# Kernel optimization log

Measured on AMD Instinct MI355X. Metric: run time of the kernel, lower is better.

The kernel has to match this reference:

```python
import jax, jax.numpy as jnp
import numpy as np
import itertools

N, F, R, O, OUT = 131072, 32, 256, 5, 100
K = 9  # 2*exp_param + 1 with exp_param=4


def setup_inputs() -> dict:
    key = jax.random.key(0)
    k1, k2, k3 = jax.random.split(key, 3)
    # binary features -> get_route(x)==1 -> categorical rule path
    x = jax.random.randint(k1, (N, F), 0, 2).astype(jnp.float32)
    # first R combinations of O feature indices out of F (itertools order, as in __init__)
    combs = np.array(list(itertools.islice(itertools.combinations(range(F), O), R)), dtype=np.int32)
    comb_space = jax.random.normal(k2, (O, R), dtype=jnp.float32)
    w_out = jax.random.normal(k3, (OUT, R), dtype=jnp.float32) * 0.05
    b_out = jnp.zeros((OUT,), jnp.float32)
    return {"x": x, "comb_space": comb_space, "w_out": w_out, "b_out": b_out,
            "comb_idx": jnp.asarray(combs)}


def reference(x, comb_space, w_out, b_out, comb_idx):
    # Fused version of the per-rule Python loop:
    # gather all rule feature subsets at once: [N, R, O]
    gathered = x[:, comb_idx]
    # per-rule dot product with its parameter vector comb_space[:, r]
    scores = jnp.einsum('nro,or->nr', gathered, comb_space)  # [N, R]
    # polyClip activation: clamp(s^k, -1, 1)
    comb_pred = jnp.clip(scores ** K, -1.0, 1.0)
    # dropout p=0.1 is identity in eval mode
    attn = jax.nn.softmax(comb_pred, axis=1)                 # [N, R]
    out = attn @ w_out.T + b_out                             # [N, OUT]
    return jax.nn.log_softmax(out, axis=1)
```

## Files before the change

### kernel.cpp

```cpp
#include <hip/hip_runtime.h>

typedef unsigned short u16;
typedef _Float16 f16;
typedef __attribute__((ext_vector_type(2))) __fp16 hf16x2;
typedef __attribute__((ext_vector_type(4))) _Float16 f16x4;
typedef __attribute__((ext_vector_type(8))) _Float16 f16x8;
typedef __attribute__((ext_vector_type(4))) float f32x4;

#define N_ROWS 131072
#define FDIM 32
#define RDIM 256
#define ODIM 5
#define NOUT 100
#define JT 7
#define WAVES 8
#define ROWS_PER_BLOCK (WAVES * 2 * 16)
#define NBLOCKS (N_ROWS / ROWS_PER_BLOCK)

__device__ __forceinline__ u16 f2h_bits(float f) {
    f16 h = (f16)f;
    union { f16 h; u16 u; } v; v.h = h;
    return v.u;
}

__device__ __forceinline__ f16x4 elemop(f32x4 cc) {
    float ev[4];
#pragma unroll
    for (int i = 0; i < 4; ++i) {
        float s = cc[i];
        float s2 = s * s, s4 = s2 * s2, s8 = s4 * s4;
        float p = __builtin_amdgcn_fmed3f(s8 * s, -1.f, 1.f);
        ev[i] = __expf(p);
    }
    union { hf16x2 h; unsigned u; } lo, hi;
    lo.h = __builtin_amdgcn_cvt_pkrtz(ev[0], ev[1]);
    hi.h = __builtin_amdgcn_cvt_pkrtz(ev[2], ev[3]);
    union { unsigned u[2]; f16x4 v; } r;
    r.u[0] = lo.u; r.u[1] = hi.u;
    return r.v;
}

__device__ __forceinline__ void epilogue2(
    const f32x4* acc0, const f32x4* acc1, const float* bv,
    int rowb0, int c15, int g, float* __restrict__ out)
{
    float rin0[4], rin1[4];
#pragma unroll
    for (int i = 0; i < 4; ++i) {
        rin0[i] = __builtin_amdgcn_rcpf(__shfl(acc0[6][i], g * 16 + 4, 64));
        rin1[i] = __builtin_amdgcn_rcpf(__shfl(acc1[6][i], g * 16 + 4, 64));
    }
    const bool v6 = (c15 < 4);
#pragma unroll
    for (int i = 0; i < 4; ++i) {
        float lg0[JT], lg1[JT];
        float se0 = 0.f, se1 = 0.f;
#pragma unroll
        for (int jt = 0; jt < 6; ++jt) {
            lg0[jt] = fmaf(acc0[jt][i], rin0[i], bv[jt]);
            lg1[jt] = fmaf(acc1[jt][i], rin1[i], bv[jt]);
            se0 += __expf(lg0[jt]);
            se1 += __expf(lg1[jt]);
        }
        lg0[6] = fmaf(acc0[6][i], rin0[i], bv[6]);
        lg1[6] = fmaf(acc1[6][i], rin1[i], bv[6]);
        se0 += v6 ? __expf(lg0[6]) : 0.f;
        se1 += v6 ? __expf(lg1[6]) : 0.f;
#pragma unroll
        for (int m = 1; m <= 8; m <<= 1) {
            se0 += __shfl_xor(se0, m, 64);
            se1 += __shfl_xor(se1, m, 64);
        }
        float lse0 = __logf(se0), lse1 = __logf(se1);
        int row0 = rowb0 + g * 4 + i;
        float* op0 = out + (size_t)row0 * NOUT;
        float* op1 = op0 + 16 * NOUT;
#pragma unroll
        for (int jt = 0; jt < 6; ++jt) {
            op0[jt * 16 + c15] = lg0[jt] - lse0;
            op1[jt * 16 + c15] = lg1[jt] - lse1;
        }
        if (v6) {
            op0[96 + c15] = lg0[6] - lse0;
            op1[96 + c15] = lg1[6] - lse1;
        }
    }
}

__global__ __launch_bounds__(WAVES * 64, 2) void hornet_main(
    const float* __restrict__ x, const float* __restrict__ cs,
    const float* __restrict__ w, const float* __restrict__ b_out,
    const int* __restrict__ ci, float* __restrict__ out)
{
    __shared__ __align__(16) u16 mf[16 * 64 * 8];
    __shared__ __align__(16) u16 wf[JT * 8 * 64 * 8];

    const int tid = threadIdx.x;
    const int lane = tid & 63;
    const int wid = tid >> 6;
    const int c15 = lane & 15, g = lane >> 4;

    const int rowb0 = blockIdx.x * ROWS_PER_BLOCK + wid * 32;
    const float* xp0 = x + (size_t)(rowb0 + c15) * FDIM + g * 8;
    float4 x0a = ((const float4*)xp0)[0];
    float4 x0b = ((const float4*)xp0)[1];
    float4 x1a = ((const float4*)(xp0 + 16 * FDIM))[0];
    float4 x1b = ((const float4*)(xp0 + 16 * FDIM))[1];

#pragma unroll
    for (int ii = 0; ii < 2; ++ii) {
        int s = tid + ii * 512;
        int l = s & 63, rt = s >> 6;
        int r = rt * 16 + (l & 15);
        int kbase = (l >> 4) * 8;
        int idx0 = ci[r * ODIM + 0], idx1 = ci[r * ODIM + 1], idx2 = ci[r * ODIM + 2];
        int idx3 = ci[r * ODIM + 3], idx4 = ci[r * ODIM + 4];
        u16 vals[8];
#pragma unroll
        for (int e = 0; e < 8; ++e) {
            int k = kbase + e;
            float v = 0.f;
            if (idx0 == k) v = cs[0 * RDIM + r];
            if (idx1 == k) v = cs[1 * RDIM + r];
            if (idx2 == k) v = cs[2 * RDIM + r];
            if (idx3 == k) v = cs[3 * RDIM + r];
            if (idx4 == k) v = cs[4 * RDIM + r];
            vals[e] = f2h_bits(v);
        }
        *(uint4*)(mf + s * 8) = *(const uint4*)vals;
    }

#pragma unroll
    for (int ii = 0; ii < 7; ++ii) {
        int s = tid + ii * 512;
        int l = s & 63, ft = s >> 6;
        int jt = ft >> 3, rtp = ft & 7;
        int j = jt * 16 + (l & 15);
        u16 vals[8];
        if (j < NOUT) {
            const float* wp = w + (size_t)j * RDIM + rtp * 32 + (l >> 4) * 4;
            float4 va = *(const float4*)wp;
            float4 vb = *(const float4*)(wp + 16);
            vals[0] = f2h_bits(va.x); vals[1] = f2h_bits(va.y);
            vals[2] = f2h_bits(va.z); vals[3] = f2h_bits(va.w);
            vals[4] = f2h_bits(vb.x); vals[5] = f2h_bits(vb.y);
            vals[6] = f2h_bits(vb.z); vals[7] = f2h_bits(vb.w);
        } else {
            u16 one = f2h_bits(1.0f);
            u16 fill = (j == NOUT) ? one : (u16)0;
#pragma unroll
            for (int e = 0; e < 8; ++e) vals[e] = fill;
        }
        *(uint4*)(wf + s * 8) = *(const uint4*)vals;
    }

    f16x8 a1_0, a1_1;
    a1_0[0] = (f16)x0a.x; a1_0[1] = (f16)x0a.y; a1_0[2] = (f16)x0a.z; a1_0[3] = (f16)x0a.w;
    a1_0[4] = (f16)x0b.x; a1_0[5] = (f16)x0b.y; a1_0[6] = (f16)x0b.z; a1_0[7] = (f16)x0b.w;
    a1_1[0] = (f16)x1a.x; a1_1[1] = (f16)x1a.y; a1_1[2] = (f16)x1a.z; a1_1[3] = (f16)x1a.w;
    a1_1[4] = (f16)x1b.x; a1_1[5] = (f16)x1b.y; a1_1[6] = (f16)x1b.z; a1_1[7] = (f16)x1b.w;

    __syncthreads();

    const f16x8* mfv = (const f16x8*)mf;
    const f16x8* wfv = (const f16x8*)wf;

    f32x4 acc0[JT], acc1[JT];
#pragma unroll
    for (int jt = 0; jt < JT; ++jt) {
        acc0[jt] = (f32x4){0.f, 0.f, 0.f, 0.f};
        acc1[jt] = (f32x4){0.f, 0.f, 0.f, 0.f};
    }

    f16x8 b1a = mfv[lane];
    f16x8 b1b = mfv[64 + lane];

#pragma unroll 1
    for (int rtp = 0; rtp < 8; ++rtp) {
        f16x8 ca = b1a, cb = b1b;
        int nrtp = (rtp + 1) & 7;
        b1a = mfv[(2 * nrtp) * 64 + lane];
        b1b = mfv[(2 * nrtp + 1) * 64 + lane];

        const f32x4 z = {0.f, 0.f, 0.f, 0.f};
        f32x4 cc0a = __builtin_amdgcn_mfma_f32_16x16x32_f16(ca, a1_0, z, 0, 0, 0);
        f32x4 cc0b = __builtin_amdgcn_mfma_f32_16x16x32_f16(cb, a1_0, z, 0, 0, 0);
        f32x4 cc1a = __builtin_amdgcn_mfma_f32_16x16x32_f16(ca, a1_1, z, 0, 0, 0);
        f32x4 cc1b = __builtin_amdgcn_mfma_f32_16x16x32_f16(cb, a1_1, z, 0, 0, 0);

        f16x4 a2lo0 = elemop(cc0a);
        f16x4 a2hi0 = elemop(cc0b);
        f16x4 a2lo1 = elemop(cc1a);
        f16x4 a2hi1 = elemop(cc1b);

        const f16x8* wrow = wfv + rtp * 64 + lane;
#pragma unroll
        for (int jt = 0; jt < JT; ++jt) {
            f16x8 b2 = wrow[jt * 8 * 64];
            f16x4 b2lo = __builtin_shufflevector(b2, b2, 0, 1, 2, 3);
            f16x4 b2hi = __builtin_shufflevector(b2, b2, 4, 5, 6, 7);
            acc0[jt] = __builtin_amdgcn_mfma_f32_16x16x16f16(a2lo0, b2lo, acc0[jt], 0, 0, 0);
            acc0[jt] = __builtin_amdgcn_mfma_f32_16x16x16f16(a2hi0, b2hi, acc0[jt], 0, 0, 0);
            acc1[jt] = __builtin_amdgcn_mfma_f32_16x16x16f16(a2lo1, b2lo, acc1[jt], 0, 0, 0);
            acc1[jt] = __builtin_amdgcn_mfma_f32_16x16x16f16(a2hi1, b2hi, acc1[jt], 0, 0, 0);
        }
    }

    float bv[JT];
#pragma unroll
    for (int jt = 0; jt < JT; ++jt) {
        int j = jt * 16 + c15;
        bv[jt] = (j < NOUT) ? b_out[j] : 0.f;
    }

    epilogue2(acc0, acc1, bv, rowb0, c15, g, out);
}

extern "C" void kernel_launch(void* const* d_in, const int* in_sizes, int n_in,
                              void* d_out, int out_size, void* d_ws, size_t ws_size,
                              hipStream_t stream) {
    const float* x  = (const float*)d_in[0];
    const float* cs = (const float*)d_in[1];
    const float* w  = (const float*)d_in[2];
    const float* b  = (const float*)d_in[3];
    const int*   ci = (const int*)d_in[4];

    hipLaunchKernelGGL(hornet_main, dim3(NBLOCKS), dim3(WAVES * 64), 0, stream,
                       x, cs, w, b, ci, (float*)d_out);
}
```

Before: 33.79 us.

## Precompute fp16 weight tables in a prep kernel and DMA them into LDS

Moves the per-block construction of the combination-matrix and output-weight fp16 tables into a separate small kernel that writes them once to workspace. The main kernel then copies the prebuilt tables into shared memory with global_load_lds direct transfers instead of gathering and converting in every block. The exp is changed to a raw v_exp_f32 (base 2), with the scores prescaled by a constant folded into the table and the clip bounds adjusted to match. MFMA sections are wrapped in s_setprio to favour matrix issue. This adds a second launch and relies on the workspace buffer.

```diff
diff --git a/kernel.cpp b/kernel.cpp
--- a/kernel.cpp
+++ b/kernel.cpp
@@ -17,105 +17,33 @@
 #define ROWS_PER_BLOCK (WAVES * 2 * 16)
 #define NBLOCKS (N_ROWS / ROWS_PER_BLOCK)
 
+#define MF_SLOTS 1024
+#define WF_SLOTS (JT * 8 * 64)
+#define TAB_SLOTS (MF_SLOTS + WF_SLOTS)
+
+#define CSCALE 1.04156363f
+#define CLIP2  1.44269504f
+
+typedef const __attribute__((address_space(1))) void gvoid;
+typedef __attribute__((address_space(3))) void lvoid;
+
 __device__ __forceinline__ u16 f2h_bits(float f) {
     f16 h = (f16)f;
     union { f16 h; u16 u; } v; v.h = h;
     return v.u;
 }
 
-__device__ __forceinline__ f16x4 elemop(f32x4 cc) {
-    float ev[4];
-#pragma unroll
-    for (int i = 0; i < 4; ++i) {
-        float s = cc[i];
-        float s2 = s * s, s4 = s2 * s2, s8 = s4 * s4;
-        float p = __builtin_amdgcn_fmed3f(s8 * s, -1.f, 1.f);
-        ev[i] = __expf(p);
-    }
-    union { hf16x2 h; unsigned u; } lo, hi;
-    lo.h = __builtin_amdgcn_cvt_pkrtz(ev[0], ev[1]);
-    hi.h = __builtin_amdgcn_cvt_pkrtz(ev[2], ev[3]);
-    union { unsigned u[2]; f16x4 v; } r;
-    r.u[0] = lo.u; r.u[1] = hi.u;
-    return r.v;
-}
-
-__device__ __forceinline__ void epilogue2(
-    const f32x4* acc0, const f32x4* acc1, const float* bv,
-    int rowb0, int c15, int g, float* __restrict__ out)
-{
-    float rin0[4], rin1[4];
-#pragma unroll
-    for (int i = 0; i < 4; ++i) {
-        rin0[i] = __builtin_amdgcn_rcpf(__shfl(acc0[6][i], g * 16 + 4, 64));
-        rin1[i] = __builtin_amdgcn_rcpf(__shfl(acc1[6][i], g * 16 + 4, 64));
-    }
-    const bool v6 = (c15 < 4);
-#pragma unroll
-    for (int i = 0; i < 4; ++i) {
-        float lg0[JT], lg1[JT];
-        float se0 = 0.f, se1 = 0.f;
-#pragma unroll
-        for (int jt = 0; jt < 6; ++jt) {
-            lg0[jt] = fmaf(acc0[jt][i], rin0[i], bv[jt]);
-            lg1[jt] = fmaf(acc1[jt][i], rin1[i], bv[jt]);
-            se0 += __expf(lg0[jt]);
-            se1 += __expf(lg1[jt]);
-        }
-        lg0[6] = fmaf(acc0[6][i], rin0[i], bv[6]);
-        lg1[6] = fmaf(acc1[6][i], rin1[i], bv[6]);
-        se0 += v6 ? __expf(lg0[6]) : 0.f;
-        se1 += v6 ? __expf(lg1[6]) : 0.f;
-#pragma unroll
-        for (int m = 1; m <= 8; m <<= 1) {
-            se0 += __shfl_xor(se0, m, 64);
-            se1 += __shfl_xor(se1, m, 64);
-        }
-        float lse0 = __logf(se0), lse1 = __logf(se1);
-        int row0 = rowb0 + g * 4 + i;
-        float* op0 = out + (size_t)row0 * NOUT;
-        float* op1 = op0 + 16 * NOUT;
-#pragma unroll
-        for (int jt = 0; jt < 6; ++jt) {
-            op0[jt * 16 + c15] = lg0[jt] - lse0;
-            op1[jt * 16 + c15] = lg1[jt] - lse1;
-        }
-        if (v6) {
-            op0[96 + c15] = lg0[6] - lse0;
-            op1[96 + c15] = lg1[6] - lse1;
-        }
-    }
-}
-
-__global__ __launch_bounds__(WAVES * 64, 2) void hornet_main(
-    const float* __restrict__ x, const float* __restrict__ cs,
-    const float* __restrict__ w, const float* __restrict__ b_out,
-    const int* __restrict__ ci, float* __restrict__ out)
-{
-    __shared__ __align__(16) u16 mf[16 * 64 * 8];
-    __shared__ __align__(16) u16 wf[JT * 8 * 64 * 8];
-
-    const int tid = threadIdx.x;
-    const int lane = tid & 63;
-    const int wid = tid >> 6;
-    const int c15 = lane & 15, g = lane >> 4;
-
-    const int rowb0 = blockIdx.x * ROWS_PER_BLOCK + wid * 32;
-    const float* xp0 = x + (size_t)(rowb0 + c15) * FDIM + g * 8;
-    float4 x0a = ((const float4*)xp0)[0];
-    float4 x0b = ((const float4*)xp0)[1];
-    float4 x1a = ((const float4*)(xp0 + 16 * FDIM))[0];
-    float4 x1b = ((const float4*)(xp0 + 16 * FDIM))[1];
-
-#pragma unroll
-    for (int ii = 0; ii < 2; ++ii) {
-        int s = tid + ii * 512;
-        int l = s & 63, rt = s >> 6;
+__global__ void build_tabs(const float* __restrict__ cs, const float* __restrict__ w,
+                           const int* __restrict__ ci, u16* __restrict__ tabs) {
+    int t = blockIdx.x * 512 + threadIdx.x;
+    if (t >= TAB_SLOTS) return;
+    u16 vals[8];
+    if (t < MF_SLOTS) {
+        int l = t & 63, rt = t >> 6;
         int r = rt * 16 + (l & 15);
         int kbase = (l >> 4) * 8;
         int idx0 = ci[r * ODIM + 0], idx1 = ci[r * ODIM + 1], idx2 = ci[r * ODIM + 2];
         int idx3 = ci[r * ODIM + 3], idx4 = ci[r * ODIM + 4];
-        u16 vals[8];
 #pragma unroll
         for (int e = 0; e < 8; ++e) {
             int k = kbase + e;
@@ -125,18 +53,13 @@
             if (idx2 == k) v = cs[2 * RDIM + r];
             if (idx3 == k) v = cs[3 * RDIM + r];
             if (idx4 == k) v = cs[4 * RDIM + r];
-            vals[e] = f2h_bits(v);
-        }
-        *(uint4*)(mf + s * 8) = *(const uint4*)vals;
-    }
-
-#pragma unroll
-    for (int ii = 0; ii < 7; ++ii) {
-        int s = tid + ii * 512;
+            vals[e] = f2h_bits(v * CSCALE);
+        }
+    } else {
+        int s = t - MF_SLOTS;
         int l = s & 63, ft = s >> 6;
         int jt = ft >> 3, rtp = ft & 7;
         int j = jt * 16 + (l & 15);
-        u16 vals[8];
         if (j < NOUT) {
             const float* wp = w + (size_t)j * RDIM + rtp * 32 + (l >> 4) * 4;
             float4 va = *(const float4*)wp;
@@ -146,12 +69,103 @@
             vals[4] = f2h_bits(vb.x); vals[5] = f2h_bits(vb.y);
             vals[6] = f2h_bits(vb.z); vals[7] = f2h_bits(vb.w);
         } else {
-            u16 one = f2h_bits(1.0f);
-            u16 fill = (j == NOUT) ? one : (u16)0;
+            u16 fill = (j == NOUT) ? f2h_bits(1.0f) : (u16)0;
 #pragma unroll
             for (int e = 0; e < 8; ++e) vals[e] = fill;
         }
-        *(uint4*)(wf + s * 8) = *(const uint4*)vals;
+    }
+    *(uint4*)(tabs + (size_t)t * 8) = *(const uint4*)vals;
+}
+
+__device__ __forceinline__ f16x4 elemop(f32x4 cc) {
+    float ev[4];
+#pragma unroll
+    for (int i = 0; i < 4; ++i) {
+        float s = cc[i];
+        float s2 = s * s, s4 = s2 * s2, s8 = s4 * s4;
+        float p = __builtin_amdgcn_fmed3f(s8 * s, -CLIP2, CLIP2);
+        float e;
+        asm("v_exp_f32 %0, %1" : "=v"(e) : "v"(p));
+        ev[i] = e;
+    }
+    union { hf16x2 h; unsigned u; } lo, hi;
+    lo.h = __builtin_amdgcn_cvt_pkrtz(ev[0], ev[1]);
+    hi.h = __builtin_amdgcn_cvt_pkrtz(ev[2], ev[3]);
+    union { unsigned u[2]; f16x4 v; } r;
+    r.u[0] = lo.u; r.u[1] = hi.u;
+    return r.v;
+}
+
+__device__ __forceinline__ void epilogue2(
+    const f32x4* acc0, const f32x4* acc1, const float* bv,
+    int rowb0, int c15, int g, float* __restrict__ out)
+{
+    float rin0[4], rin1[4];
+#pragma unroll
+    for (int i = 0; i < 4; ++i) {
+        rin0[i] = __builtin_amdgcn_rcpf(__shfl(acc0[6][i], g * 16 + 4, 64));
+        rin1[i] = __builtin_amdgcn_rcpf(__shfl(acc1[6][i], g * 16 + 4, 64));
+    }
+    const bool v6 = (c15 < 4);
+#pragma unroll
+    for (int i = 0; i < 4; ++i) {
+        float lg0[JT], lg1[JT];
+        float se0 = 0.f, se1 = 0.f;
+#pragma unroll
+        for (int jt = 0; jt < 6; ++jt) {
+            lg0[jt] = fmaf(acc0[jt][i], rin0[i], bv[jt]);
+            lg1[jt] = fmaf(acc1[jt][i], rin1[i], bv[jt]);
+            se0 += __expf(lg0[jt]);
+            se1 += __expf(lg1[jt]);
+        }
+        lg0[6] = fmaf(acc0[6][i], rin0[i], bv[6]);
+        lg1[6] = fmaf(acc1[6][i], rin1[i], bv[6]);
+        se0 += v6 ? __expf(lg0[6]) : 0.f;
+        se1 += v6 ? __expf(lg1[6]) : 0.f;
+#pragma unroll
+        for (int m = 1; m <= 8; m <<= 1) {
+            se0 += __shfl_xor(se0, m, 64);
+            se1 += __shfl_xor(se1, m, 64);
+        }
+        float lse0 = __logf(se0), lse1 = __logf(se1);
+        int row0 = rowb0 + g * 4 + i;
+        float* op0 = out + (size_t)row0 * NOUT;
+        float* op1 = op0 + 16 * NOUT;
+#pragma unroll
+        for (int jt = 0; jt < 6; ++jt) {
+            op0[jt * 16 + c15] = lg0[jt] - lse0;
+            op1[jt * 16 + c15] = lg1[jt] - lse1;
+        }
+        if (v6) {
+            op0[96 + c15] = lg0[6] - lse0;
+            op1[96 + c15] = lg1[6] - lse1;
+        }
+    }
+}
+
+__global__ __launch_bounds__(WAVES * 64, 2) void hornet_main(
+    const float* __restrict__ x, const u16* __restrict__ tabs,
+    const float* __restrict__ b_out, float* __restrict__ out)
+{
+    __shared__ __align__(16) u16 tab[TAB_SLOTS * 8];
+
+    const int tid = threadIdx.x;
+    const int lane = tid & 63;
+    const int wid = tid >> 6;
+    const int c15 = lane & 15, g = lane >> 4;
+
+    const int rowb0 = blockIdx.x * ROWS_PER_BLOCK + wid * 32;
+    const float* xp0 = x + (size_t)(rowb0 + c15) * FDIM + g * 8;
+    float4 x0a = ((const float4*)xp0)[0];
+    float4 x0b = ((const float4*)xp0)[1];
+    float4 x1a = ((const float4*)(xp0 + 16 * FDIM))[0];
+    float4 x1b = ((const float4*)(xp0 + 16 * FDIM))[1];
+
+#pragma unroll
+    for (int i = 0; i < 9; ++i) {
+        const u16* gp = tabs + (size_t)(tid + i * 512) * 8;
+        u16* lp = tab + (size_t)(wid * 64 + i * 512) * 8;
+        __builtin_amdgcn_global_load_lds((gvoid*)gp, (lvoid*)lp, 16, 0, 0);
     }
 
     f16x8 a1_0, a1_1;
@@ -162,8 +176,8 @@
 
     __syncthreads();
 
-    const f16x8* mfv = (const f16x8*)mf;
-    const f16x8* wfv = (const f16x8*)wf;
+    const f16x8* mfv = (const f16x8*)tab;
+    const f16x8* wfv = (const f16x8*)(tab + MF_SLOTS * 8);
 
     f32x4 acc0[JT], acc1[JT];
 #pragma unroll
@@ -183,10 +197,12 @@
         b1b = mfv[(2 * nrtp + 1) * 64 + lane];
 
         const f32x4 z = {0.f, 0.f, 0.f, 0.f};
+        __builtin_amdgcn_s_setprio(1);
         f32x4 cc0a = __builtin_amdgcn_mfma_f32_16x16x32_f16(ca, a1_0, z, 0, 0, 0);
         f32x4 cc0b = __builtin_amdgcn_mfma_f32_16x16x32_f16(cb, a1_0, z, 0, 0, 0);
         f32x4 cc1a = __builtin_amdgcn_mfma_f32_16x16x32_f16(ca, a1_1, z, 0, 0, 0);
         f32x4 cc1b = __builtin_amdgcn_mfma_f32_16x16x32_f16(cb, a1_1, z, 0, 0, 0);
+        __builtin_amdgcn_s_setprio(0);
 
         f16x4 a2lo0 = elemop(cc0a);
         f16x4 a2hi0 = elemop(cc0b);
@@ -194,6 +210,7 @@
         f16x4 a2hi1 = elemop(cc1b);
 
         const f16x8* wrow = wfv + rtp * 64 + lane;
+        __builtin_amdgcn_s_setprio(1);
 #pragma unroll
         for (int jt = 0; jt < JT; ++jt) {
             f16x8 b2 = wrow[jt * 8 * 64];
@@ -204,6 +221,7 @@
             acc1[jt] = __builtin_amdgcn_mfma_f32_16x16x16f16(a2lo1, b2lo, acc1[jt], 0, 0, 0);
             acc1[jt] = __builtin_amdgcn_mfma_f32_16x16x16f16(a2hi1, b2hi, acc1[jt], 0, 0, 0);
         }
+        __builtin_amdgcn_s_setprio(0);
     }
 
     float bv[JT];
@@ -225,6 +243,9 @@
     const float* b  = (const float*)d_in[3];
     const int*   ci = (const int*)d_in[4];
 
+    u16* tabs = (u16*)d_ws;
+
+    hipLaunchKernelGGL(build_tabs, dim3(9), dim3(512), 0, stream, cs, w, ci, tabs);
     hipLaunchKernelGGL(hornet_main, dim3(NBLOCKS), dim3(WAVES * 64), 0, stream,
-                       x, cs, w, b, ci, (float*)d_out);
-}
+                       x, tabs, b, (float*)d_out);
+}
```

Result: faster. 31.48 us (-6.8%).
